# Kernel tuning notes

Measured on AMD Instinct MI355X. Metric: run time of the kernel, lower is better.

## Reference

```python
import jax, jax.numpy as jnp
import numpy as np

NEG_SLOPE = 0.1  # LeakyReLU slope used throughout CamLiFlow

def _batch_gather(feat, idx):
    # feat: [B, C, N], idx: [B, N, K] -> [B, C, N, K]
    return jax.vmap(lambda f, i: f[:, i])(feat, idx)

def _point_conv(xyz, feat, idx, wn_w, wn_b, lin_w, lin_b):
    # xyz: [B,3,N], feat: [B,C,N], idx: [B,N,K]
    B, _, N = xyz.shape
    feat_cat = jnp.concatenate([xyz, feat], axis=1)            # [B, C+3, N]
    knn_xyz = _batch_gather(xyz, idx)                          # [B, 3, N, K]
    rel = knn_xyz - xyz[:, :, :, None]                         # centered neighbor coords
    # weight net: 1x1 conv 3 -> 8 + LeakyReLU
    w = jax.nn.leaky_relu(
        jnp.einsum('oc,bcnk->bonk', wn_w, rel) + wn_b[None, :, None, None],
        NEG_SLOPE)                                             # [B, 8, N, K]
    knn_feat = _batch_gather(feat_cat, idx)                    # [B, C+3, N, K]
    agg = jnp.einsum('bonk,bcnk->bnoc', w, knn_feat)           # [B, N, 8, C+3]
    out = agg.reshape(B, N, -1) @ lin_w.T + lin_b              # [B, N, out]
    return jax.nn.leaky_relu(out, NEG_SLOPE).transpose(0, 2, 1)  # [B, out, N]

def _conv1d(x, w, b):
    # 1x1 Conv1d: x [B,C,N], w [O,C], b [O]
    return jnp.einsum('oc,bcn->bon', w, x) + b[None, :, None]

def setup_inputs() -> dict:
    key = jax.random.key(0)
    ks = jax.random.split(key, 16)
    B, N, K = 4, 8192, 16
    C0, C1, C2, C3 = 128, 128, 128, 64
    s = 0.02
    inp = {
        'xyz': jax.random.normal(ks[0], (B, 3, N), jnp.float32),
        'feat': jax.random.normal(ks[1], (B, C0, N), jnp.float32),
        'knn_indices': jax.random.randint(ks[2], (B, N, K), 0, N),
        # point_conv1
        'wn1_w': jax.random.normal(ks[3], (8, 3), jnp.float32) * s,
        'wn1_b': jnp.zeros((8,), jnp.float32),
        'lin1_w': jax.random.normal(ks[4], (C1, 8 * (C0 + 3)), jnp.float32) * s,
        'lin1_b': jnp.zeros((C1,), jnp.float32),
        # point_conv2
        'wn2_w': jax.random.normal(ks[5], (8, 3), jnp.float32) * s,
        'wn2_b': jnp.zeros((8,), jnp.float32),
        'lin2_w': jax.random.normal(ks[6], (C2, 8 * (C1 + 3)), jnp.float32) * s,
        'lin2_b': jnp.zeros((C2,), jnp.float32),
        # MLP1d: C2 -> C2 -> C3 (1x1 convs + LeakyReLU)
        'm1_w': jax.random.normal(ks[7], (C2, C2), jnp.float32) * s,
        'm1_b': jnp.zeros((C2,), jnp.float32),
        'm2_w': jax.random.normal(ks[8], (C3, C2), jnp.float32) * s,
        'm2_b': jnp.zeros((C3,), jnp.float32),
        # conv_last: C3 -> 3
        'cl_w': jax.random.normal(ks[9], (3, C3), jnp.float32) * s,
        'cl_b': jnp.zeros((3,), jnp.float32),
    }
    return inp

def reference(xyz, feat, knn_indices, wn1_w, wn1_b, lin1_w, lin1_b,
              wn2_w, wn2_b, lin2_w, lin2_b, m1_w, m1_b, m2_w, m2_b,
              cl_w, cl_b):
    f = _point_conv(xyz, feat, knn_indices, wn1_w, wn1_b, lin1_w, lin1_b)  # [B,128,N]
    f = _point_conv(xyz, f, knn_indices, wn2_w, wn2_b, lin2_w, lin2_b)     # [B,128,N]
    f = jax.nn.leaky_relu(_conv1d(f, m1_w, m1_b), NEG_SLOPE)
    flow_feat = jax.nn.leaky_relu(_conv1d(f, m2_w, m2_b), NEG_SLOPE)       # [B,64,N]
    flow = _conv1d(flow_feat, cl_w, cl_b)                                  # [B,3,N]
    return flow_feat, flow
```

## Files before the change

kernel.cpp:

```cpp
#include <hip/hip_runtime.h>

typedef __bf16 bf16x8 __attribute__((ext_vector_type(8)));
typedef float  f32x4  __attribute__((ext_vector_type(4)));
typedef float  f32x2  __attribute__((ext_vector_type(2)));
typedef unsigned int u32x4 __attribute__((ext_vector_type(4)));
typedef unsigned short u16;

#define NPTS 8192
#define NB   4
#define KNN  16
#define ROW  136
#define CF   131
#define JBLK 136
#define NSTEP 34
#define AGG_STRIDE 1096
#define HALF_U16 8704
#define WOFF  17408
#define RBOFF 19456
#define SMEM_U16 19712
#define F2T   0
#define H1OFF 2304
#define FFOFF 4608
#define NEG 0.1f

#define WAITVM(n) __builtin_amdgcn_s_waitcnt(0x0F70 | (n))
#define SB() __builtin_amdgcn_sched_barrier(0)

__device__ __forceinline__ float b2f(u16 h) {
    return __uint_as_float(((unsigned int)h) << 16);
}
__device__ __forceinline__ u16 f2bf(float f) {
    unsigned int u = __float_as_uint(f);
    return (u16)((u + 0x8000u) >> 16);
}
__device__ __forceinline__ void dma16(const u16* g, u16* l) {
    __builtin_amdgcn_global_load_lds(
        (const __attribute__((address_space(1))) void*)g,
        (__attribute__((address_space(3))) void*)l, 16, 0, 0);
}
__device__ __forceinline__ float lrelu(float v) {
    return (v < 0.0f) ? NEG * v : v;
}

__global__ __launch_bounds__(256) void pack_all(
    const float* __restrict__ xyz, const float* __restrict__ feat,
    u16* __restrict__ fcT1, u16* __restrict__ fcT2, float* __restrict__ xyzF,
    const float* __restrict__ l1, const float* __restrict__ l2,
    const float* __restrict__ w1, const float* __restrict__ w2,
    u16* __restrict__ o1, u16* __restrict__ o2,
    u16* __restrict__ o3, u16* __restrict__ o4)
{
    int t = threadIdx.x;
    if (blockIdx.x < 512) {
        __shared__ u16 tile[CF * 65];
        int blk = blockIdx.x;
        int b = blk >> 7;
        int n0 = (blk & 127) << 6;
        int nn = t & 63;
        #pragma unroll 1
        for (int c = (t >> 6); c < CF; c += 4) {
            float v;
            if (c < 3) v = xyz[(size_t)b * 3 * NPTS + (size_t)c * NPTS + n0 + nn];
            else       v = feat[(size_t)b * 128 * NPTS + (size_t)(c - 3) * NPTS + n0 + nn];
            tile[c * 65 + nn] = f2bf(v);
            if (c < 3) xyzF[((size_t)b * NPTS + n0 + nn) * 4 + c] = v;
        }
        __syncthreads();
        #pragma unroll 1
        for (int e = t; e < 64 * 17; e += 256) {
            int r = e / 17;
            int u = e - r * 17;
            int c0 = u * 8;
            unsigned int w[4];
            #pragma unroll
            for (int i = 0; i < 4; i++) {
                int ca = c0 + 2 * i, cb = ca + 1;
                unsigned lo = (ca < CF) ? (unsigned)tile[ca * 65 + r] : 0u;
                unsigned hi = (cb < CF) ? (unsigned)tile[cb * 65 + r] : 0u;
                w[i] = lo | (hi << 16);
            }
            size_t row = (size_t)b * NPTS + n0 + r;
            *(u32x4*)(fcT1 + row * ROW + c0) = (u32x4){w[0], w[1], w[2], w[3]};
            if (u == 0 || u == 16)
                *(u32x4*)(fcT2 + row * ROW + c0) = (u32x4){w[0], w[1], w[2], w[3]};
        }
    } else {
        int blk = blockIdx.x - 512;
        const float* w; u16* out; int O, Cin, remap, b0;
        if (blk < 68)       { w = l1; out = o1; O = 128; Cin = 1048; remap = 1; b0 = 0; }
        else if (blk < 136) { w = l2; out = o2; O = 128; Cin = 1048; remap = 1; b0 = 68; }
        else if (blk < 144) { w = w1; out = o3; O = 128; Cin = 128;  remap = 0; b0 = 136; }
        else                { w = w2; out = o4; O = 64;  Cin = 128;  remap = 0; b0 = 144; }
        int T = O >> 4;
        int tid = (blk - b0) * 256 + t;
        int l = tid & 63;
        int st = tid >> 6;
        int tt = st % T;
        int s = st / T;
        int o = tt * 16 + (l & 15);
        int kb = s * 32 + ((l >> 4) * 8);
        #pragma unroll 1
        for (int j = 0; j < 8; j++) {
            int kh = kb + j;
            u16 v = 0;
            if (remap) {
                int jj = kh / JBLK, cc = kh - jj * JBLK;
                if (cc < CF) v = f2bf(w[(size_t)o * Cin + jj * CF + cc]);
            } else {
                if (kh < Cin) v = f2bf(w[(size_t)o * Cin + kh]);
            }
            out[(size_t)tid * 8 + j] = v;
        }
    }
}

__device__ __forceinline__ void pc_core(
    u16* __restrict__ smem,
    const u16* __restrict__ fcT, const float* __restrict__ xyzF,
    const int* __restrict__ knn, const float* __restrict__ wn_w,
    const float* __restrict__ wn_b, const u16* __restrict__ lwP,
    int pt0, int b, int n0, f32x4& acc1o, f32x4& acc2o)
{
    int t = threadIdx.x;
    int wv = t >> 6, lane = t & 63;
    int p = t >> 4, cl = t & 15;
    u16* rb16 = smem + RBOFF;

    {
        size_t rowC = (size_t)b * NPTS + n0 + p;
        int idxv = knn[rowC * KNN + cl];
        int rb = b * NPTS + idxv;
        rb16[p * 16 + cl] = (u16)rb;
        f32x4 cx = *(const f32x4*)(xyzF + rowC * 4);
        f32x4 nx = *(const f32x4*)(xyzF + (size_t)rb * 4);
        float rx = nx[0] - cx[0], ry = nx[1] - cx[1], rz = nx[2] - cx[2];
        unsigned int wp[4];
        #pragma unroll
        for (int jj = 0; jj < 4; jj++) {
            float a0 = lrelu(wn_w[(2 * jj) * 3 + 0] * rx + wn_w[(2 * jj) * 3 + 1] * ry +
                             wn_w[(2 * jj) * 3 + 2] * rz + wn_b[2 * jj]);
            float a1 = lrelu(wn_w[(2 * jj + 1) * 3 + 0] * rx + wn_w[(2 * jj + 1) * 3 + 1] * ry +
                             wn_w[(2 * jj + 1) * 3 + 2] * rz + wn_b[2 * jj + 1]);
            wp[jj] = (unsigned)f2bf(a0) | ((unsigned)f2bf(a1) << 16);
        }
        *(u32x4*)(smem + WOFF + (p * 16 + cl) * 8) = (u32x4){wp[0], wp[1], wp[2], wp[3]};
    }

    f32x2 acc[4][8];
    float acct[8];
    #pragma unroll
    for (int i = 0; i < 4; i++)
        #pragma unroll
        for (int j = 0; j < 8; j++) acc[i][j] = (f32x2){0.f, 0.f};
    #pragma unroll
    for (int j = 0; j < 8; j++) acct[j] = 0.f;

    int rbidx[5], remu[5], ldso[5];
    #pragma unroll
    for (int i = 0; i < 5; i++) {
        int slot = i * 64 + lane;
        int rl = slot / 17;
        int rem = slot - rl * 17;
        int pp = wv * 4 + (rl >> 2);
        int kk = rl & 3;
        rbidx[i] = pp * 16 + kk;
        remu[i] = rem * 8;
        ldso[i] = (pp * 4 + kk) * 136 + rem * 8;
    }

    auto issue = [&](int c) {
        int h = c & 1;
        #pragma unroll
        for (int i = 0; i < 5; i++) {
            if (i < 4 || lane < 16) {
                int rb = (int)rb16[rbidx[i] + c * 4];
                dma16(fcT + (size_t)rb * ROW + remu[i],
                      smem + h * HALF_U16 + ldso[i]);
            }
        }
    };
    auto consume = [&](int c) {
        int h = c & 1;
        const u16* rpb = smem + h * HALF_U16 + p * (4 * 136);
        const u16* wpb = smem + WOFF + (p * 16 + c * 4) * 8;
        #pragma unroll 2
        for (int kk = 0; kk < 4; kk++) {
            u32x4 rv = *(const u32x4*)(rpb + kk * 136 + cl * 8);
            float tl = (cl < 3) ? b2f(rpb[kk * 136 + 128 + cl]) : 0.0f;
            u32x4 wv4 = *(const u32x4*)(wpb + kk * 8);
            f32x2 v[4];
            float wr[8];
            #pragma unroll
            for (int i = 0; i < 4; i++) {
                unsigned int u = rv[i];
                v[i] = (f32x2){__uint_as_float(u << 16),
                               __uint_as_float(u & 0xFFFF0000u)};
                unsigned int uw = wv4[i];
                wr[2 * i]     = __uint_as_float(uw << 16);
                wr[2 * i + 1] = __uint_as_float(uw & 0xFFFF0000u);
            }
            #pragma unroll
            for (int j = 0; j < 8; j++) {
                f32x2 w2 = (f32x2){wr[j], wr[j]};
                #pragma unroll
                for (int i = 0; i < 4; i++) acc[i][j] += v[i] * w2;
                acct[j] += tl * wr[j];
            }
        }
    };

    issue(0); issue(1);
    #pragma unroll 1
    for (int c = 0; c < 2; c++) {
        WAITVM(5); SB(); consume(c); SB(); issue(c + 2); SB();
    }
    WAITVM(5); SB(); consume(2); SB();
    WAITVM(0); SB(); consume(3);
    __syncthreads();

    {
        #pragma unroll
        for (int j = 0; j < 8; j++) {
            unsigned int o[4];
            #pragma unroll
            for (int i = 0; i < 4; i++) {
                unsigned int lo = f2bf(acc[i][j].x);
                unsigned int hi = f2bf(acc[i][j].y);
                o[i] = lo | (hi << 16);
            }
            *(u32x4*)(smem + p * AGG_STRIDE + j * JBLK + cl * 8) =
                (u32x4){o[0], o[1], o[2], o[3]};
        }
        if (cl < 3) {
            #pragma unroll
            for (int j = 0; j < 8; j++)
                smem[p * AGG_STRIDE + j * JBLK + 128 + cl] = f2bf(acct[j]);
        }
        if (cl < 5) {
            #pragma unroll
            for (int j = 0; j < 8; j++)
                smem[p * AGG_STRIDE + j * JBLK + CF + cl] = 0;
        }
    }
    __syncthreads();

    {
        int m = lane & 15, quad = lane >> 4;
        f32x4 a1 = {0.f, 0.f, 0.f, 0.f};
        f32x4 a2 = {0.f, 0.f, 0.f, 0.f};
        #pragma unroll 4
        for (int s = 0; s < NSTEP; s++) {
            u32x4 av = *(const u32x4*)(smem + m * AGG_STRIDE + s * 32 + quad * 8);
            u32x4 bv1 = *(const u32x4*)(lwP + (((size_t)(s * 8 + wv) * 64 + lane) << 3));
            u32x4 bv2 = *(const u32x4*)(lwP + (((size_t)(s * 8 + wv + 4) * 64 + lane) << 3));
            a1 = __builtin_amdgcn_mfma_f32_16x16x32_bf16(
                __builtin_bit_cast(bf16x8, av), __builtin_bit_cast(bf16x8, bv1), a1, 0, 0, 0);
            a2 = __builtin_amdgcn_mfma_f32_16x16x32_bf16(
                __builtin_bit_cast(bf16x8, av), __builtin_bit_cast(bf16x8, bv2), a2, 0, 0, 0);
        }
        acc1o = a1; acc2o = a2;
    }
}

__global__ __launch_bounds__(256) void pc_kernel0(
    const u16* __restrict__ fcT, const float* __restrict__ xyzF,
    const int* __restrict__ knn, const float* __restrict__ wn_w,
    const float* __restrict__ wn_b, const u16* __restrict__ lwP,
    const float* __restrict__ lin_b, u16* __restrict__ out)
{
    __shared__ __align__(16) u16 smem[SMEM_U16];
    int t = threadIdx.x;
    int wv = t >> 6, lane = t & 63;
    int pt0 = blockIdx.x * 16;
    int b = pt0 >> 13;
    int n0 = pt0 & (NPTS - 1);
    f32x4 a1, a2;
    pc_core(smem, fcT, xyzF, knn, wn_w, wn_b, lwP, pt0, b, n0, a1, a2);
    int col = lane & 15, quad = lane >> 4;
    int o1 = wv * 16 + col, o2 = (wv + 4) * 16 + col;
    float bb1 = lin_b[o1], bb2 = lin_b[o2];
    #pragma unroll
    for (int r = 0; r < 4; r++) {
        int prow = pt0 + quad * 4 + r;
        out[(size_t)prow * ROW + 3 + o1] = f2bf(lrelu(a1[r] + bb1));
        out[(size_t)prow * ROW + 3 + o2] = f2bf(lrelu(a2[r] + bb2));
    }
}

__global__ __launch_bounds__(256) void pc_kernel1(
    const u16* __restrict__ fcT, const float* __restrict__ xyzF,
    const int* __restrict__ knn, const float* __restrict__ wn_w,
    const float* __restrict__ wn_b, const u16* __restrict__ lwP,
    const float* __restrict__ lin_b,
    const u16* __restrict__ m1P, const float* __restrict__ m1_b,
    const u16* __restrict__ m2P, const float* __restrict__ m2_b,
    const float* __restrict__ cl_w, const float* __restrict__ cl_b,
    float* __restrict__ dout)
{
    __shared__ __align__(16) u16 smem[SMEM_U16];
    int t = threadIdx.x;
    int wv = t >> 6, lane = t & 63;
    int pt0 = blockIdx.x * 16;
    int b = pt0 >> 13;
    int n0 = pt0 & (NPTS - 1);
    f32x4 a1, a2;
    pc_core(smem, fcT, xyzF, knn, wn_w, wn_b, lwP, pt0, b, n0, a1, a2);
    int col = lane & 15, quad = lane >> 4;
    int m = lane & 15;

    {
        int o1 = wv * 16 + col, o2 = (wv + 4) * 16 + col;
        float bb1 = lin_b[o1], bb2 = lin_b[o2];
        __syncthreads();
        #pragma unroll
        for (int r = 0; r < 4; r++) {
            int pr = quad * 4 + r;
            smem[F2T + pr * 128 + o1] = f2bf(lrelu(a1[r] + bb1));
            smem[F2T + pr * 128 + o2] = f2bf(lrelu(a2[r] + bb2));
        }
    }
    __syncthreads();

    {
        f32x4 g1 = {0.f, 0.f, 0.f, 0.f};
        f32x4 g2 = {0.f, 0.f, 0.f, 0.f};
        #pragma unroll 2
        for (int s = 0; s < 4; s++) {
            u32x4 av = *(const u32x4*)(smem + F2T + m * 128 + s * 32 + quad * 8);
            u32x4 bv1 = *(const u32x4*)(m1P + (((size_t)(s * 8 + wv) * 64 + lane) << 3));
            u32x4 bv2 = *(const u32x4*)(m1P + (((size_t)(s * 8 + wv + 4) * 64 + lane) << 3));
            g1 = __builtin_amdgcn_mfma_f32_16x16x32_bf16(
                __builtin_bit_cast(bf16x8, av), __builtin_bit_cast(bf16x8, bv1), g1, 0, 0, 0);
            g2 = __builtin_amdgcn_mfma_f32_16x16x32_bf16(
                __builtin_bit_cast(bf16x8, av), __builtin_bit_cast(bf16x8, bv2), g2, 0, 0, 0);
        }
        int o1 = wv * 16 + col, o2 = (wv + 4) * 16 + col;
        float bb1 = m1_b[o1], bb2 = m1_b[o2];
        #pragma unroll
        for (int r = 0; r < 4; r++) {
            int pr = quad * 4 + r;
            smem[H1OFF + pr * 136 + o1] = f2bf(lrelu(g1[r] + bb1));
            smem[H1OFF + pr * 136 + o2] = f2bf(lrelu(g2[r] + bb2));
        }
    }
    __syncthreads();

    {
        float* ffp = (float*)(smem + FFOFF);
        f32x4 g = {0.f, 0.f, 0.f, 0.f};
        #pragma unroll 2
        for (int s = 0; s < 4; s++) {
            u32x4 av = *(const u32x4*)(smem + H1OFF + m * 136 + s * 32 + quad * 8);
            u32x4 bv = *(const u32x4*)(m2P + (((size_t)(s * 4 + wv) * 64 + lane) << 3));
            g = __builtin_amdgcn_mfma_f32_16x16x32_bf16(
                __builtin_bit_cast(bf16x8, av), __builtin_bit_cast(bf16x8, bv), g, 0, 0, 0);
        }
        int o = wv * 16 + col;
        float bb = m2_b[o];
        #pragma unroll
        for (int r = 0; r < 4; r++) {
            int pr = quad * 4 + r;
            float v = lrelu(g[r] + bb);
            dout[((size_t)b * 64 + o) * NPTS + n0 + pr] = v;
            ffp[pr * 68 + o] = v;
        }
    }
    __syncthreads();

    if (t < 48) {
        float* ffp = (float*)(smem + FFOFF);
        int pp = t & 15, oo = t >> 4;
        float a = cl_b[oo];
        #pragma unroll 8
        for (int i = 0; i < 64; i++)
            a += cl_w[oo * 64 + i] * ffp[pp * 68 + i];
        dout[(size_t)NB * 64 * NPTS + ((size_t)b * 3 + oo) * NPTS + n0 + pp] = a;
    }
}

extern "C" void kernel_launch(void* const* d_in, const int* in_sizes, int n_in,
                              void* d_out, int out_size, void* d_ws, size_t ws_size,
                              hipStream_t stream) {
    const float* xyz   = (const float*)d_in[0];
    const float* feat  = (const float*)d_in[1];
    const int*   knn   = (const int*)d_in[2];
    const float* wn1_w = (const float*)d_in[3];
    const float* wn1_b = (const float*)d_in[4];
    const float* lin1w = (const float*)d_in[5];
    const float* lin1b = (const float*)d_in[6];
    const float* wn2_w = (const float*)d_in[7];
    const float* wn2_b = (const float*)d_in[8];
    const float* lin2w = (const float*)d_in[9];
    const float* lin2b = (const float*)d_in[10];
    const float* m1_w  = (const float*)d_in[11];
    const float* m1_b  = (const float*)d_in[12];
    const float* m2_w  = (const float*)d_in[13];
    const float* m2_b  = (const float*)d_in[14];
    const float* cl_w  = (const float*)d_in[15];
    const float* cl_b  = (const float*)d_in[16];
    float* out = (float*)d_out;

    char* ws = (char*)d_ws;
    const size_t BN = (size_t)NB * NPTS;
    u16*   fcT1 = (u16*)(ws);
    u16*   fcT2 = (u16*)(ws + 8912896);
    float* xyzF = (float*)(ws + 17825792);
    u16*   lw1P = (u16*)(ws + 18350080);
    u16*   lw2P = (u16*)(ws + 18628608);
    u16*   m1P  = (u16*)(ws + 18907136);
    u16*   m2P  = (u16*)(ws + 18939904);

    (void)in_sizes; (void)n_in; (void)out_size; (void)ws_size;

    pack_all<<<dim3(660), dim3(256), 0, stream>>>(
        xyz, feat, fcT1, fcT2, xyzF,
        lin1w, lin2w, m1_w, m2_w, lw1P, lw2P, m1P, m2P);
    pc_kernel0<<<dim3(BN / 16), dim3(256), 0, stream>>>(
        fcT1, xyzF, knn, wn1_w, wn1_b, lw1P, lin1b, fcT2);
    pc_kernel1<<<dim3(BN / 16), dim3(256), 0, stream>>>(
        fcT2, xyzF, knn, wn2_w, wn2_b, lw2P, lin2b,
        m1P, m1_b, m2P, m2_b, cl_w, cl_b, out);
}
```

Baseline: 194.3 us.

## Fuse pack and both point-conv stages into one persistent kernel with grid barriers

Replaces the three launches (pack, point conv 1, point conv 2 plus MLP) with a single persistent kernel of 512 blocks. The stages are separated by a software grid-wide barrier built on global atomics, and each block loops over point tiles with a stride of 512. The aim is to remove launch gaps and tail effects between the kernels. In exchange, occupancy is limited to the persistent grid, the pack stage loses its parallel overlap, and the spin barrier relies on all blocks being co-resident, which risks deadlock if they are not.

```diff
diff --git a/kernel.cpp b/kernel.cpp
--- a/kernel.cpp
+++ b/kernel.cpp
@@ -22,6 +22,7 @@
 #define H1OFF 2304
 #define FFOFF 4608
 #define NEG 0.1f
+#define NBLK 512
 
 #define WAITVM(n) __builtin_amdgcn_s_waitcnt(0x0F70 | (n))
 #define SB() __builtin_amdgcn_sched_barrier(0)
@@ -42,76 +43,31 @@
     return (v < 0.0f) ? NEG * v : v;
 }
 
-__global__ __launch_bounds__(256) void pack_all(
-    const float* __restrict__ xyz, const float* __restrict__ feat,
-    u16* __restrict__ fcT1, u16* __restrict__ fcT2, float* __restrict__ xyzF,
-    const float* __restrict__ l1, const float* __restrict__ l2,
-    const float* __restrict__ w1, const float* __restrict__ w2,
-    u16* __restrict__ o1, u16* __restrict__ o2,
-    u16* __restrict__ o3, u16* __restrict__ o4)
-{
-    int t = threadIdx.x;
-    if (blockIdx.x < 512) {
-        __shared__ u16 tile[CF * 65];
-        int blk = blockIdx.x;
-        int b = blk >> 7;
-        int n0 = (blk & 127) << 6;
-        int nn = t & 63;
-        #pragma unroll 1
-        for (int c = (t >> 6); c < CF; c += 4) {
-            float v;
-            if (c < 3) v = xyz[(size_t)b * 3 * NPTS + (size_t)c * NPTS + n0 + nn];
-            else       v = feat[(size_t)b * 128 * NPTS + (size_t)(c - 3) * NPTS + n0 + nn];
-            tile[c * 65 + nn] = f2bf(v);
-            if (c < 3) xyzF[((size_t)b * NPTS + n0 + nn) * 4 + c] = v;
-        }
-        __syncthreads();
-        #pragma unroll 1
-        for (int e = t; e < 64 * 17; e += 256) {
-            int r = e / 17;
-            int u = e - r * 17;
-            int c0 = u * 8;
-            unsigned int w[4];
-            #pragma unroll
-            for (int i = 0; i < 4; i++) {
-                int ca = c0 + 2 * i, cb = ca + 1;
-                unsigned lo = (ca < CF) ? (unsigned)tile[ca * 65 + r] : 0u;
-                unsigned hi = (cb < CF) ? (unsigned)tile[cb * 65 + r] : 0u;
-                w[i] = lo | (hi << 16);
-            }
-            size_t row = (size_t)b * NPTS + n0 + r;
-            *(u32x4*)(fcT1 + row * ROW + c0) = (u32x4){w[0], w[1], w[2], w[3]};
-            if (u == 0 || u == 16)
-                *(u32x4*)(fcT2 + row * ROW + c0) = (u32x4){w[0], w[1], w[2], w[3]};
-        }
-    } else {
-        int blk = blockIdx.x - 512;
-        const float* w; u16* out; int O, Cin, remap, b0;
-        if (blk < 68)       { w = l1; out = o1; O = 128; Cin = 1048; remap = 1; b0 = 0; }
-        else if (blk < 136) { w = l2; out = o2; O = 128; Cin = 1048; remap = 1; b0 = 68; }
-        else if (blk < 144) { w = w1; out = o3; O = 128; Cin = 128;  remap = 0; b0 = 136; }
-        else                { w = w2; out = o4; O = 64;  Cin = 128;  remap = 0; b0 = 144; }
-        int T = O >> 4;
-        int tid = (blk - b0) * 256 + t;
-        int l = tid & 63;
-        int st = tid >> 6;
-        int tt = st % T;
-        int s = st / T;
-        int o = tt * 16 + (l & 15);
-        int kb = s * 32 + ((l >> 4) * 8);
-        #pragma unroll 1
-        for (int j = 0; j < 8; j++) {
-            int kh = kb + j;
-            u16 v = 0;
-            if (remap) {
-                int jj = kh / JBLK, cc = kh - jj * JBLK;
-                if (cc < CF) v = f2bf(w[(size_t)o * Cin + jj * CF + cc]);
-            } else {
-                if (kh < Cin) v = f2bf(w[(size_t)o * Cin + kh]);
-            }
-            out[(size_t)tid * 8 + j] = v;
-        }
-    }
+__device__ unsigned g_cnt = 0;
+__device__ unsigned g_gen = 0;
+
+__device__ __forceinline__ void global_barrier() {
+    __syncthreads();
+    __threadfence();
+    if (threadIdx.x == 0) {
+        unsigned g = __hip_atomic_load(&g_gen, __ATOMIC_RELAXED,
+                                       __HIP_MEMORY_SCOPE_AGENT);
+        unsigned a = __hip_atomic_fetch_add(&g_cnt, 1u, __ATOMIC_ACQ_REL,
+                                            __HIP_MEMORY_SCOPE_AGENT);
+        if (a == (unsigned)(NBLK - 1)) {
+            __hip_atomic_store(&g_cnt, 0u, __ATOMIC_RELAXED,
+                               __HIP_MEMORY_SCOPE_AGENT);
+            __hip_atomic_store(&g_gen, g + 1u, __ATOMIC_RELEASE,
+                               __HIP_MEMORY_SCOPE_AGENT);
+        } else {
+            while (__hip_atomic_load(&g_gen, __ATOMIC_ACQUIRE,
+                                     __HIP_MEMORY_SCOPE_AGENT) == g) {
+                __builtin_amdgcn_s_sleep(8);
+            }
+        }
+        __threadfence();
+    }
+    __syncthreads();
 }
 
 __device__ __forceinline__ void pc_core(
@@ -262,119 +218,192 @@
     }
 }
 
-__global__ __launch_bounds__(256) void pc_kernel0(
-    const u16* __restrict__ fcT, const float* __restrict__ xyzF,
-    const int* __restrict__ knn, const float* __restrict__ wn_w,
-    const float* __restrict__ wn_b, const u16* __restrict__ lwP,
-    const float* __restrict__ lin_b, u16* __restrict__ out)
+__global__ __launch_bounds__(256, 2) void fused_all(
+    const float* __restrict__ xyz, const float* __restrict__ feat,
+    const int* __restrict__ knn,
+    const float* __restrict__ wn1_w, const float* __restrict__ wn1_b,
+    const float* __restrict__ lin1w, const float* __restrict__ lin1b,
+    const float* __restrict__ wn2_w, const float* __restrict__ wn2_b,
+    const float* __restrict__ lin2w, const float* __restrict__ lin2b,
+    const float* __restrict__ m1_w, const float* __restrict__ m1_b,
+    const float* __restrict__ m2_w, const float* __restrict__ m2_b,
+    const float* __restrict__ cl_w, const float* __restrict__ cl_b,
+    float* __restrict__ dout,
+    u16* __restrict__ fcT1, u16* __restrict__ fcT2, float* __restrict__ xyzF,
+    u16* __restrict__ lw1P, u16* __restrict__ lw2P,
+    u16* __restrict__ m1P, u16* __restrict__ m2P)
 {
     __shared__ __align__(16) u16 smem[SMEM_U16];
     int t = threadIdx.x;
-    int wv = t >> 6, lane = t & 63;
-    int pt0 = blockIdx.x * 16;
-    int b = pt0 >> 13;
-    int n0 = pt0 & (NPTS - 1);
-    f32x4 a1, a2;
-    pc_core(smem, fcT, xyzF, knn, wn_w, wn_b, lwP, pt0, b, n0, a1, a2);
-    int col = lane & 15, quad = lane >> 4;
-    int o1 = wv * 16 + col, o2 = (wv + 4) * 16 + col;
-    float bb1 = lin_b[o1], bb2 = lin_b[o2];
-    #pragma unroll
-    for (int r = 0; r < 4; r++) {
-        int prow = pt0 + quad * 4 + r;
-        out[(size_t)prow * ROW + 3 + o1] = f2bf(lrelu(a1[r] + bb1));
-        out[(size_t)prow * ROW + 3 + o2] = f2bf(lrelu(a2[r] + bb2));
-    }
-}
-
-__global__ __launch_bounds__(256) void pc_kernel1(
-    const u16* __restrict__ fcT, const float* __restrict__ xyzF,
-    const int* __restrict__ knn, const float* __restrict__ wn_w,
-    const float* __restrict__ wn_b, const u16* __restrict__ lwP,
-    const float* __restrict__ lin_b,
-    const u16* __restrict__ m1P, const float* __restrict__ m1_b,
-    const u16* __restrict__ m2P, const float* __restrict__ m2_b,
-    const float* __restrict__ cl_w, const float* __restrict__ cl_b,
-    float* __restrict__ dout)
-{
-    __shared__ __align__(16) u16 smem[SMEM_U16];
-    int t = threadIdx.x;
-    int wv = t >> 6, lane = t & 63;
-    int pt0 = blockIdx.x * 16;
-    int b = pt0 >> 13;
-    int n0 = pt0 & (NPTS - 1);
-    f32x4 a1, a2;
-    pc_core(smem, fcT, xyzF, knn, wn_w, wn_b, lwP, pt0, b, n0, a1, a2);
-    int col = lane & 15, quad = lane >> 4;
-    int m = lane & 15;
-
-    {
-        int o1 = wv * 16 + col, o2 = (wv + 4) * 16 + col;
-        float bb1 = lin_b[o1], bb2 = lin_b[o2];
+    int blk = blockIdx.x;
+
+    {
+        u16* tile = smem;
+        int b = blk >> 7;
+        int n0 = (blk & 127) << 6;
+        int nn = t & 63;
+        #pragma unroll 1
+        for (int c = (t >> 6); c < CF; c += 4) {
+            float v;
+            if (c < 3) v = xyz[(size_t)b * 3 * NPTS + (size_t)c * NPTS + n0 + nn];
+            else       v = feat[(size_t)b * 128 * NPTS + (size_t)(c - 3) * NPTS + n0 + nn];
+            tile[c * 65 + nn] = f2bf(v);
+            if (c < 3) xyzF[((size_t)b * NPTS + n0 + nn) * 4 + c] = v;
+        }
         __syncthreads();
-        #pragma unroll
-        for (int r = 0; r < 4; r++) {
-            int pr = quad * 4 + r;
-            smem[F2T + pr * 128 + o1] = f2bf(lrelu(a1[r] + bb1));
-            smem[F2T + pr * 128 + o2] = f2bf(lrelu(a2[r] + bb2));
-        }
-    }
-    __syncthreads();
-
-    {
-        f32x4 g1 = {0.f, 0.f, 0.f, 0.f};
-        f32x4 g2 = {0.f, 0.f, 0.f, 0.f};
-        #pragma unroll 2
-        for (int s = 0; s < 4; s++) {
-            u32x4 av = *(const u32x4*)(smem + F2T + m * 128 + s * 32 + quad * 8);
-            u32x4 bv1 = *(const u32x4*)(m1P + (((size_t)(s * 8 + wv) * 64 + lane) << 3));
-            u32x4 bv2 = *(const u32x4*)(m1P + (((size_t)(s * 8 + wv + 4) * 64 + lane) << 3));
-            g1 = __builtin_amdgcn_mfma_f32_16x16x32_bf16(
-                __builtin_bit_cast(bf16x8, av), __builtin_bit_cast(bf16x8, bv1), g1, 0, 0, 0);
-            g2 = __builtin_amdgcn_mfma_f32_16x16x32_bf16(
-                __builtin_bit_cast(bf16x8, av), __builtin_bit_cast(bf16x8, bv2), g2, 0, 0, 0);
-        }
-        int o1 = wv * 16 + col, o2 = (wv + 4) * 16 + col;
-        float bb1 = m1_b[o1], bb2 = m1_b[o2];
-        #pragma unroll
-        for (int r = 0; r < 4; r++) {
-            int pr = quad * 4 + r;
-            smem[H1OFF + pr * 136 + o1] = f2bf(lrelu(g1[r] + bb1));
-            smem[H1OFF + pr * 136 + o2] = f2bf(lrelu(g2[r] + bb2));
-        }
-    }
-    __syncthreads();
-
-    {
-        float* ffp = (float*)(smem + FFOFF);
-        f32x4 g = {0.f, 0.f, 0.f, 0.f};
-        #pragma unroll 2
-        for (int s = 0; s < 4; s++) {
-            u32x4 av = *(const u32x4*)(smem + H1OFF + m * 136 + s * 32 + quad * 8);
-            u32x4 bv = *(const u32x4*)(m2P + (((size_t)(s * 4 + wv) * 64 + lane) << 3));
-            g = __builtin_amdgcn_mfma_f32_16x16x32_bf16(
-                __builtin_bit_cast(bf16x8, av), __builtin_bit_cast(bf16x8, bv), g, 0, 0, 0);
-        }
-        int o = wv * 16 + col;
-        float bb = m2_b[o];
-        #pragma unroll
-        for (int r = 0; r < 4; r++) {
-            int pr = quad * 4 + r;
-            float v = lrelu(g[r] + bb);
-            dout[((size_t)b * 64 + o) * NPTS + n0 + pr] = v;
-            ffp[pr * 68 + o] = v;
-        }
-    }
-    __syncthreads();
-
-    if (t < 48) {
-        float* ffp = (float*)(smem + FFOFF);
-        int pp = t & 15, oo = t >> 4;
-        float a = cl_b[oo];
-        #pragma unroll 8
-        for (int i = 0; i < 64; i++)
-            a += cl_w[oo * 64 + i] * ffp[pp * 68 + i];
-        dout[(size_t)NB * 64 * NPTS + ((size_t)b * 3 + oo) * NPTS + n0 + pp] = a;
+        #pragma unroll 1
+        for (int e = t; e < 64 * 17; e += 256) {
+            int r = e / 17;
+            int u = e - r * 17;
+            int c0 = u * 8;
+            unsigned int w[4];
+            #pragma unroll
+            for (int i = 0; i < 4; i++) {
+                int ca = c0 + 2 * i, cb = ca + 1;
+                unsigned lo = (ca < CF) ? (unsigned)tile[ca * 65 + r] : 0u;
+                unsigned hi = (cb < CF) ? (unsigned)tile[cb * 65 + r] : 0u;
+                w[i] = lo | (hi << 16);
+            }
+            size_t row = (size_t)b * NPTS + n0 + r;
+            *(u32x4*)(fcT1 + row * ROW + c0) = (u32x4){w[0], w[1], w[2], w[3]};
+            if (u == 0 || u == 16)
+                *(u32x4*)(fcT2 + row * ROW + c0) = (u32x4){w[0], w[1], w[2], w[3]};
+        }
+        if (blk < 148) {
+            const float* w; u16* out; int O, Cin, remap, b0;
+            if (blk < 68)       { w = lin1w; out = lw1P; O = 128; Cin = 1048; remap = 1; b0 = 0; }
+            else if (blk < 136) { w = lin2w; out = lw2P; O = 128; Cin = 1048; remap = 1; b0 = 68; }
+            else if (blk < 144) { w = m1_w;  out = m1P;  O = 128; Cin = 128;  remap = 0; b0 = 136; }
+            else                { w = m2_w;  out = m2P;  O = 64;  Cin = 128;  remap = 0; b0 = 144; }
+            int T = O >> 4;
+            int tid = (blk - b0) * 256 + t;
+            int l = tid & 63;
+            int st = tid >> 6;
+            int tt = st % T;
+            int s = st / T;
+            int o = tt * 16 + (l & 15);
+            int kb = s * 32 + ((l >> 4) * 8);
+            #pragma unroll 1
+            for (int j = 0; j < 8; j++) {
+                int kh = kb + j;
+                u16 v = 0;
+                if (remap) {
+                    int jj = kh / JBLK, cc = kh - jj * JBLK;
+                    if (cc < CF) v = f2bf(w[(size_t)o * Cin + jj * CF + cc]);
+                } else {
+                    if (kh < Cin) v = f2bf(w[(size_t)o * Cin + kh]);
+                }
+                out[(size_t)tid * 8 + j] = v;
+            }
+        }
+    }
+    global_barrier();
+
+    {
+        int wv = t >> 6, lane = t & 63;
+        int col = lane & 15, quad = lane >> 4;
+        #pragma unroll 1
+        for (int tl = blk; tl < (NB * NPTS / 16); tl += NBLK) {
+            int pt0 = tl * 16;
+            int b = pt0 >> 13;
+            int n0 = pt0 & (NPTS - 1);
+            f32x4 a1, a2;
+            pc_core(smem, fcT1, xyzF, knn, wn1_w, wn1_b, lw1P, pt0, b, n0, a1, a2);
+            int o1 = wv * 16 + col, o2 = (wv + 4) * 16 + col;
+            float bb1 = lin1b[o1], bb2 = lin1b[o2];
+            #pragma unroll
+            for (int r = 0; r < 4; r++) {
+                int prow = pt0 + quad * 4 + r;
+                fcT2[(size_t)prow * ROW + 3 + o1] = f2bf(lrelu(a1[r] + bb1));
+                fcT2[(size_t)prow * ROW + 3 + o2] = f2bf(lrelu(a2[r] + bb2));
+            }
+            __syncthreads();
+        }
+    }
+    global_barrier();
+
+    {
+        int wv = t >> 6, lane = t & 63;
+        int col = lane & 15, quad = lane >> 4;
+        int m = lane & 15;
+        #pragma unroll 1
+        for (int tl = blk; tl < (NB * NPTS / 16); tl += NBLK) {
+            int pt0 = tl * 16;
+            int b = pt0 >> 13;
+            int n0 = pt0 & (NPTS - 1);
+            f32x4 a1, a2;
+            pc_core(smem, fcT2, xyzF, knn, wn2_w, wn2_b, lw2P, pt0, b, n0, a1, a2);
+
+            {
+                int o1 = wv * 16 + col, o2 = (wv + 4) * 16 + col;
+                float bb1 = lin2b[o1], bb2 = lin2b[o2];
+                __syncthreads();
+                #pragma unroll
+                for (int r = 0; r < 4; r++) {
+                    int pr = quad * 4 + r;
+                    smem[F2T + pr * 128 + o1] = f2bf(lrelu(a1[r] + bb1));
+                    smem[F2T + pr * 128 + o2] = f2bf(lrelu(a2[r] + bb2));
+                }
+            }
+            __syncthreads();
+
+            {
+                f32x4 g1 = {0.f, 0.f, 0.f, 0.f};
+                f32x4 g2 = {0.f, 0.f, 0.f, 0.f};
+                #pragma unroll 2
+                for (int s = 0; s < 4; s++) {
+                    u32x4 av = *(const u32x4*)(smem + F2T + m * 128 + s * 32 + quad * 8);
+                    u32x4 bv1 = *(const u32x4*)(m1P + (((size_t)(s * 8 + wv) * 64 + lane) << 3));
+                    u32x4 bv2 = *(const u32x4*)(m1P + (((size_t)(s * 8 + wv + 4) * 64 + lane) << 3));
+                    g1 = __builtin_amdgcn_mfma_f32_16x16x32_bf16(
+                        __builtin_bit_cast(bf16x8, av), __builtin_bit_cast(bf16x8, bv1), g1, 0, 0, 0);
+                    g2 = __builtin_amdgcn_mfma_f32_16x16x32_bf16(
+                        __builtin_bit_cast(bf16x8, av), __builtin_bit_cast(bf16x8, bv2), g2, 0, 0, 0);
+                }
+                int o1 = wv * 16 + col, o2 = (wv + 4) * 16 + col;
+                float bb1 = m1_b[o1], bb2 = m1_b[o2];
+                #pragma unroll
+                for (int r = 0; r < 4; r++) {
+                    int pr = quad * 4 + r;
+                    smem[H1OFF + pr * 136 + o1] = f2bf(lrelu(g1[r] + bb1));
+                    smem[H1OFF + pr * 136 + o2] = f2bf(lrelu(g2[r] + bb2));
+                }
+            }
+            __syncthreads();
+
+            {
+                float* ffp = (float*)(smem + FFOFF);
+                f32x4 g = {0.f, 0.f, 0.f, 0.f};
+                #pragma unroll 2
+                for (int s = 0; s < 4; s++) {
+                    u32x4 av = *(const u32x4*)(smem + H1OFF + m * 136 + s * 32 + quad * 8);
+                    u32x4 bv = *(const u32x4*)(m2P + (((size_t)(s * 4 + wv) * 64 + lane) << 3));
+                    g = __builtin_amdgcn_mfma_f32_16x16x32_bf16(
+                        __builtin_bit_cast(bf16x8, av), __builtin_bit_cast(bf16x8, bv), g, 0, 0, 0);
+                }
+                int o = wv * 16 + col;
+                float bb = m2_b[o];
+                #pragma unroll
+                for (int r = 0; r < 4; r++) {
+                    int pr = quad * 4 + r;
+                    float v = lrelu(g[r] + bb);
+                    dout[((size_t)b * 64 + o) * NPTS + n0 + pr] = v;
+                    ffp[pr * 68 + o] = v;
+                }
+            }
+            __syncthreads();
+
+            if (t < 48) {
+                float* ffp = (float*)(smem + FFOFF);
+                int pp = t & 15, oo = t >> 4;
+                float a = cl_b[oo];
+                #pragma unroll 8
+                for (int i = 0; i < 64; i++)
+                    a += cl_w[oo * 64 + i] * ffp[pp * 68 + i];
+                dout[(size_t)NB * 64 * NPTS + ((size_t)b * 3 + oo) * NPTS + n0 + pp] = a;
+            }
+            __syncthreads();
+        }
     }
 }
 
@@ -401,7 +430,6 @@
     float* out = (float*)d_out;
 
     char* ws = (char*)d_ws;
-    const size_t BN = (size_t)NB * NPTS;
     u16*   fcT1 = (u16*)(ws);
     u16*   fcT2 = (u16*)(ws + 8912896);
     float* xyzF = (float*)(ws + 17825792);
@@ -412,12 +440,11 @@
 
     (void)in_sizes; (void)n_in; (void)out_size; (void)ws_size;
 
-    pack_all<<<dim3(660), dim3(256), 0, stream>>>(
-        xyz, feat, fcT1, fcT2, xyzF,
-        lin1w, lin2w, m1_w, m2_w, lw1P, lw2P, m1P, m2P);
-    pc_kernel0<<<dim3(BN / 16), dim3(256), 0, stream>>>(
-        fcT1, xyzF, knn, wn1_w, wn1_b, lw1P, lin1b, fcT2);
-    pc_kernel1<<<dim3(BN / 16), dim3(256), 0, stream>>>(
-        fcT2, xyzF, knn, wn2_w, wn2_b, lw2P, lin2b,
-        m1P, m1_b, m2P, m2_b, cl_w, cl_b, out);
-}
+    fused_all<<<dim3(NBLK), dim3(256), 0, stream>>>(
+        xyz, feat, knn,
+        wn1_w, wn1_b, lin1w, lin1b,
+        wn2_w, wn2_b, lin2w, lin2b,
+        m1_w, m1_b, m2_w, m2_b,
+        cl_w, cl_b, out,
+        fcT1, fcT2, xyzF, lw1P, lw2P, m1P, m2P);
+}
```

After: 553.7 us. 2.85x slower.
